# Kernel optimization log

Hardware: AMD Instinct MI355X
Metric: run time of the kernel (lower is better)

Reference implementation:

```python
import jax, jax.numpy as jnp
import numpy as np

DIM = 64


def setup_inputs() -> dict:
    key = jax.random.key(0)
    k1, k2, k3 = jax.random.split(key, 3)
    x = jax.random.normal(k1, (65536, DIM), dtype=jnp.float32)
    alpha = jax.random.uniform(k2, (), dtype=jnp.float32)
    beta = jax.random.uniform(k3, (), dtype=jnp.float32)
    return {"x": x, "alpha": alpha, "beta": beta}


def reference(x, alpha, beta):
    # Static upper-triangular index pairs (i < j), same as triu(...,1).nonzero()
    iu, ju = jnp.triu_indices(DIM, k=1)
    e = jnp.exp(-alpha * x)                 # [B, dim]
    # a[b, p] = exp(-alpha*x_i) - exp(-alpha*x_j) for each pair p=(i,j), i<j.
    # Equivalent to building the dense [B, dim, dim] tensor and gathering triu.
    a = e[..., iu] - e[..., ju]             # [B, dim*(dim-1)/2]
    log_vander = jnp.sum(jnp.log(jnp.abs(a)), axis=-1)  # [B]
    return 2.0 * (-beta * jnp.sum(x, axis=-1) + log_vander)
```

## Files before the change

kernel.cpp:

```cpp
#include <hip/hip_runtime.h>

#define DIM 64

__global__ __launch_bounds__(256) void vander_kernel(
    const float* __restrict__ x, const float* __restrict__ alpha,
    const float* __restrict__ beta, float* __restrict__ out, int nrows) {
  int row = blockIdx.x * blockDim.x + threadIdx.x;
  if (row >= nrows) return;

  const float c = -alpha[0] * 1.44269504088896340736f;
  const float b = beta[0];

  const float4* xr = reinterpret_cast<const float4*>(x) + row * (DIM / 4);

  float e[DIM];
  float xs = 0.f;
#pragma unroll
  for (int k = 0; k < DIM / 4; ++k) {
    float4 v = xr[k];
    xs += (v.x + v.y) + (v.z + v.w);
    e[4 * k + 0] = __builtin_amdgcn_exp2f(c * v.x);
    e[4 * k + 1] = __builtin_amdgcn_exp2f(c * v.y);
    e[4 * k + 2] = __builtin_amdgcn_exp2f(c * v.z);
    e[4 * k + 3] = __builtin_amdgcn_exp2f(c * v.w);
  }

  float accs[4] = {0.f, 0.f, 0.f, 0.f};
  float buf[4];
  int cnt = 0, g = 0;
#pragma unroll
  for (int i = 0; i < DIM; ++i) {
#pragma unroll
    for (int j = i + 1; j < DIM; ++j) {
      buf[cnt++] = e[i] - e[j];
      if (cnt == 4) {
        float p = (buf[0] * buf[1]) * (buf[2] * buf[3]);
        float ap = __builtin_fmaxf(__builtin_fabsf(p), 1e-37f);
        accs[g & 3] += __builtin_amdgcn_logf(ap);
        ++g;
        cnt = 0;
      }
    }
  }
  float lv = (accs[0] + accs[1]) + (accs[2] + accs[3]);
  out[row] = 2.0f * (-b * xs + 0.69314718055994530942f * lv);
}

extern "C" void kernel_launch(void* const* d_in, const int* in_sizes, int n_in,
                              void* d_out, int out_size, void* d_ws, size_t ws_size,
                              hipStream_t stream) {
  const float* x = (const float*)d_in[0];
  const float* alpha = (const float*)d_in[1];
  const float* beta = (const float*)d_in[2];
  float* out = (float*)d_out;
  int nrows = in_sizes[0] / DIM;
  int block = 256;
  int grid = (nrows + block - 1) / block;
  hipLaunchKernelGGL(vander_kernel, dim3(grid), dim3(block), 0, stream,
                     x, alpha, beta, out, nrows);
}
```

Measured before the change: 76.57 us.

## Split each row's pair products across eight waves with folded triangular slices

```diff
diff --git a/kernel.cpp b/kernel.cpp
--- a/kernel.cpp
+++ b/kernel.cpp
@@ -2,17 +2,54 @@
 
 #define DIM 64
 
-__global__ __launch_bounds__(256) void vander_kernel(
+template <int A, int T>
+__device__ __forceinline__ float pdiff(const float (&e)[DIM]) {
+  constexpr int N1 = 63 - A;
+  constexpr int I = (T < N1) ? A : 62 - A;
+  constexpr int J = (T < N1) ? (A + 1 + T) : T;
+  return e[I] - e[J];
+}
+
+template <int A, int T, int NT>
+__device__ __forceinline__ void groups(const float (&e)[DIM], float& a0, float& a1) {
+  if constexpr (T < NT) {
+    float d0 = pdiff<A, T + 0>(e);
+    float d1 = pdiff<A, T + 1>(e);
+    float d2 = pdiff<A, T + 2>(e);
+    float d3 = pdiff<A, T + 3>(e);
+    float p = (d0 * d1) * (d2 * d3);
+    float ap = __builtin_fmaxf(__builtin_fabsf(p), 1e-37f);
+    if constexpr ((T & 4) == 0) {
+      a0 += __builtin_amdgcn_logf(ap);
+    } else {
+      a1 += __builtin_amdgcn_logf(ap);
+    }
+    groups<A, T + 4, NT>(e, a0, a1);
+  }
+}
+
+template <int W>
+__device__ __forceinline__ void do_slice(const float (&e)[DIM], float& a0, float& a1) {
+  groups<W, 0, 64>(e, a0, a1);
+  groups<W + 8, 0, 64>(e, a0, a1);
+  groups<W + 16, 0, 64>(e, a0, a1);
+  if constexpr (W + 24 < 31) {
+    groups<W + 24, 0, 64>(e, a0, a1);
+  } else {
+    groups<31, 0, 32>(e, a0, a1);
+  }
+}
+
+__global__ __launch_bounds__(512) void vander_kernel(
     const float* __restrict__ x, const float* __restrict__ alpha,
-    const float* __restrict__ beta, float* __restrict__ out, int nrows) {
-  int row = blockIdx.x * blockDim.x + threadIdx.x;
-  if (row >= nrows) return;
+    const float* __restrict__ beta, float* __restrict__ out) {
+  const int lane = threadIdx.x & 63;
+  const int w = threadIdx.x >> 6;
+  const int row = blockIdx.x * 64 + lane;
 
   const float c = -alpha[0] * 1.44269504088896340736f;
-  const float b = beta[0];
 
   const float4* xr = reinterpret_cast<const float4*>(x) + row * (DIM / 4);
-
   float e[DIM];
   float xs = 0.f;
 #pragma unroll
@@ -25,25 +62,27 @@
     e[4 * k + 3] = __builtin_amdgcn_exp2f(c * v.w);
   }
 
-  float accs[4] = {0.f, 0.f, 0.f, 0.f};
-  float buf[4];
-  int cnt = 0, g = 0;
-#pragma unroll
-  for (int i = 0; i < DIM; ++i) {
-#pragma unroll
-    for (int j = i + 1; j < DIM; ++j) {
-      buf[cnt++] = e[i] - e[j];
-      if (cnt == 4) {
-        float p = (buf[0] * buf[1]) * (buf[2] * buf[3]);
-        float ap = __builtin_fmaxf(__builtin_fabsf(p), 1e-37f);
-        accs[g & 3] += __builtin_amdgcn_logf(ap);
-        ++g;
-        cnt = 0;
-      }
-    }
+  float a0 = 0.f, a1 = 0.f;
+  switch (w) {
+    case 0: do_slice<0>(e, a0, a1); break;
+    case 1: do_slice<1>(e, a0, a1); break;
+    case 2: do_slice<2>(e, a0, a1); break;
+    case 3: do_slice<3>(e, a0, a1); break;
+    case 4: do_slice<4>(e, a0, a1); break;
+    case 5: do_slice<5>(e, a0, a1); break;
+    case 6: do_slice<6>(e, a0, a1); break;
+    default: do_slice<7>(e, a0, a1); break;
   }
-  float lv = (accs[0] + accs[1]) + (accs[2] + accs[3]);
-  out[row] = 2.0f * (-b * xs + 0.69314718055994530942f * lv);
+
+  __shared__ float ps[8][64];
+  ps[w][lane] = a0 + a1;
+  __syncthreads();
+
+  if (w == 0) {
+    float lv = ((ps[0][lane] + ps[1][lane]) + (ps[2][lane] + ps[3][lane])) +
+               ((ps[4][lane] + ps[5][lane]) + (ps[6][lane] + ps[7][lane]));
+    out[row] = 2.0f * (-beta[0] * xs + 0.69314718055994530942f * lv);
+  }
 }
 
 extern "C" void kernel_launch(void* const* d_in, const int* in_sizes, int n_in,
@@ -54,8 +93,7 @@
   const float* beta = (const float*)d_in[2];
   float* out = (float*)d_out;
   int nrows = in_sizes[0] / DIM;
-  int block = 256;
-  int grid = (nrows + block - 1) / block;
-  hipLaunchKernelGGL(vander_kernel, dim3(grid), dim3(block), 0, stream,
-                     x, alpha, beta, out, nrows);
+  int grid = nrows / 64;
+  hipLaunchKernelGGL(vander_kernel, dim3(grid), dim3(512), 0, stream,
+                     x, alpha, beta, out);
 }
```

Result: slower. 84.71 us (+10.6%).

## Split each row's pair-products across 8 waves via LDS tiles

Applied to the files above, without the earlier changes.

```diff
diff --git a/kernel.cpp b/kernel.cpp
--- a/kernel.cpp
+++ b/kernel.cpp
@@ -1,49 +1,125 @@
 #include <hip/hip_runtime.h>
 
-#define DIM 64
+#define STRIDE 66
 
-__global__ __launch_bounds__(256) void vander_kernel(
+typedef float v2f __attribute__((ext_vector_type(2)));
+
+__device__ __forceinline__ float lg(float p) {
+  return __builtin_amdgcn_logf(__builtin_fmaxf(__builtin_fabsf(p), 1e-37f));
+}
+
+__device__ __forceinline__ void load8(const float* p, float* r) {
+#pragma unroll
+  for (int k = 0; k < 4; ++k) {
+    float2 v = *reinterpret_cast<const float2*>(p + 2 * k);
+    r[2 * k] = v.x;
+    r[2 * k + 1] = v.y;
+  }
+}
+
+__device__ __forceinline__ void off8(const float* ei, const float* ej,
+                                     float& a0, float& a1) {
+  v2f e01 = {ej[0], ej[1]}, e23 = {ej[2], ej[3]};
+  v2f e45 = {ej[4], ej[5]}, e67 = {ej[6], ej[7]};
+#pragma unroll
+  for (int i = 0; i < 8; ++i) {
+    v2f b = {ei[i], ei[i]};
+    v2f d0 = b - e01, d1 = b - e23, d2 = b - e45, d3 = b - e67;
+    v2f p = d0 * d1, q = d2 * d3;
+    a0 += lg(p.x * p.y);
+    a1 += lg(q.x * q.y);
+  }
+}
+
+__device__ __forceinline__ void diag8(const float* e, float& a0, float& a1) {
+  a0 += lg(((e[0] - e[1]) * (e[0] - e[2])) * ((e[0] - e[3]) * (e[0] - e[4])));
+  a1 += lg(((e[0] - e[5]) * (e[0] - e[6])) * ((e[0] - e[7]) * (e[1] - e[2])));
+  a0 += lg(((e[1] - e[3]) * (e[1] - e[4])) * ((e[1] - e[5]) * (e[1] - e[6])));
+  a1 += lg(((e[1] - e[7]) * (e[2] - e[3])) * ((e[2] - e[4]) * (e[2] - e[5])));
+  a0 += lg(((e[2] - e[6]) * (e[2] - e[7])) * ((e[3] - e[4]) * (e[3] - e[5])));
+  a1 += lg(((e[3] - e[6]) * (e[3] - e[7])) * ((e[4] - e[5]) * (e[4] - e[6])));
+  a0 += lg(((e[4] - e[7]) * (e[5] - e[6])) * ((e[5] - e[7]) * (e[6] - e[7])));
+}
+
+__global__ __launch_bounds__(512, 6) void vander_kernel(
     const float* __restrict__ x, const float* __restrict__ alpha,
-    const float* __restrict__ beta, float* __restrict__ out, int nrows) {
-  int row = blockIdx.x * blockDim.x + threadIdx.x;
-  if (row >= nrows) return;
+    const float* __restrict__ beta, float* __restrict__ out) {
+  __shared__ float e_lds[64 * STRIDE];
+  __shared__ float xsum[512];
+  __shared__ float ps[512];
 
+  const int tid = threadIdx.x;
   const float c = -alpha[0] * 1.44269504088896340736f;
-  const float b = beta[0];
 
-  const float4* xr = reinterpret_cast<const float4*>(x) + row * (DIM / 4);
+  {
+    const float4* xp =
+        reinterpret_cast<const float4*>(x + (size_t)blockIdx.x * 4096 + tid * 8);
+    float4 u = xp[0], v = xp[1];
+    float ev[8];
+    ev[0] = __builtin_amdgcn_exp2f(c * u.x);
+    ev[1] = __builtin_amdgcn_exp2f(c * u.y);
+    ev[2] = __builtin_amdgcn_exp2f(c * u.z);
+    ev[3] = __builtin_amdgcn_exp2f(c * u.w);
+    ev[4] = __builtin_amdgcn_exp2f(c * v.x);
+    ev[5] = __builtin_amdgcn_exp2f(c * v.y);
+    ev[6] = __builtin_amdgcn_exp2f(c * v.z);
+    ev[7] = __builtin_amdgcn_exp2f(c * v.w);
+    float* ew = &e_lds[(tid >> 3) * STRIDE + (tid & 7) * 8];
+#pragma unroll
+    for (int k = 0; k < 4; ++k) {
+      float2 t;
+      t.x = ev[2 * k];
+      t.y = ev[2 * k + 1];
+      *reinterpret_cast<float2*>(ew + 2 * k) = t;
+    }
+    xsum[tid] = ((u.x + u.y) + (u.z + u.w)) + ((v.x + v.y) + (v.z + v.w));
+  }
+  __syncthreads();
 
-  float e[DIM];
-  float xs = 0.f;
+  const int lane = tid & 63;
+  const int w = tid >> 6;
+  const float* myrow = &e_lds[lane * STRIDE];
+  float a0 = 0.f, a1 = 0.f;
+
+  if (w < 6) {
+    int ti = (w < 3) ? 0 : ((w < 5) ? 1 : 2);
+    int tj = (w == 0) ? 1 : (w == 1) ? 2 : (w == 2) ? 3 : (w == 3) ? 2 : 3;
+    float ei[16], ej[16];
+    load8(myrow + ti * 16, ei);
+    load8(myrow + ti * 16 + 8, ei + 8);
+    load8(myrow + tj * 16, ej);
+    load8(myrow + tj * 16 + 8, ej + 8);
+    off8(ei, ej, a0, a1);
+    off8(ei, ej + 8, a0, a1);
+    off8(ei + 8, ej, a0, a1);
+    off8(ei + 8, ej + 8, a0, a1);
+  } else {
+    int d = (w - 6) * 2;
 #pragma unroll
-  for (int k = 0; k < DIM / 4; ++k) {
-    float4 v = xr[k];
-    xs += (v.x + v.y) + (v.z + v.w);
-    e[4 * k + 0] = __builtin_amdgcn_exp2f(c * v.x);
-    e[4 * k + 1] = __builtin_amdgcn_exp2f(c * v.y);
-    e[4 * k + 2] = __builtin_amdgcn_exp2f(c * v.z);
-    e[4 * k + 3] = __builtin_amdgcn_exp2f(c * v.w);
-  }
-
-  float accs[4] = {0.f, 0.f, 0.f, 0.f};
-  float buf[4];
-  int cnt = 0, g = 0;
-#pragma unroll
-  for (int i = 0; i < DIM; ++i) {
-#pragma unroll
-    for (int j = i + 1; j < DIM; ++j) {
-      buf[cnt++] = e[i] - e[j];
-      if (cnt == 4) {
-        float p = (buf[0] * buf[1]) * (buf[2] * buf[3]);
-        float ap = __builtin_fmaxf(__builtin_fabsf(p), 1e-37f);
-        accs[g & 3] += __builtin_amdgcn_logf(ap);
-        ++g;
-        cnt = 0;
-      }
+    for (int t = 0; t < 2; ++t) {
+      float ei[16];
+      load8(myrow + (d + t) * 16, ei);
+      load8(myrow + (d + t) * 16 + 8, ei + 8);
+      off8(ei, ei + 8, a0, a1);
+      diag8(ei, a0, a1);
+      diag8(ei + 8, a0, a1);
     }
   }
-  float lv = (accs[0] + accs[1]) + (accs[2] + accs[3]);
-  out[row] = 2.0f * (-b * xs + 0.69314718055994530942f * lv);
+  ps[lane * 8 + w] = a0 + a1;
+  __syncthreads();
+
+  if (w == 0) {
+    const float* pp = &ps[lane * 8];
+    const float* xq = &xsum[lane * 8];
+    float lv = 0.f, xs = 0.f;
+#pragma unroll
+    for (int k = 0; k < 8; ++k) {
+      lv += pp[k];
+      xs += xq[k];
+    }
+    out[blockIdx.x * 64 + lane] =
+        2.0f * (-beta[0] * xs + 0.69314718055994530942f * lv);
+  }
 }
 
 extern "C" void kernel_launch(void* const* d_in, const int* in_sizes, int n_in,
@@ -53,9 +129,8 @@
   const float* alpha = (const float*)d_in[1];
   const float* beta = (const float*)d_in[2];
   float* out = (float*)d_out;
-  int nrows = in_sizes[0] / DIM;
-  int block = 256;
-  int grid = (nrows + block - 1) / block;
-  hipLaunchKernelGGL(vander_kernel, dim3(grid), dim3(block), 0, stream,
-                     x, alpha, beta, out, nrows);
+  int nrows = in_sizes[0] / 64;
+  int grid = nrows / 64;
+  hipLaunchKernelGGL(vander_kernel, dim3(grid), dim3(512), 0, stream,
+                     x, alpha, beta, out);
 }
```

New measurement: 71.62 us. 1.07x faster.

## Split each row's pairwise work across four waves via LDS-staged exponentials

Applied to the files above, without the earlier changes.

```diff
diff --git a/kernel.cpp b/kernel.cpp
--- a/kernel.cpp
+++ b/kernel.cpp
@@ -1,49 +1,120 @@
 #include <hip/hip_runtime.h>
 
-#define DIM 64
+#define STRIDE 66
+
+typedef float v2f __attribute__((ext_vector_type(2)));
+
+__constant__ unsigned char CI[28] = {0,0,0,0,0,0,0, 1,1,1,1,1,1, 2,2,2,2,2, 3,3,3,3, 4,4,4, 5,5, 6};
+__constant__ unsigned char CJ[28] = {1,2,3,4,5,6,7, 2,3,4,5,6,7, 3,4,5,6,7, 4,5,6,7, 5,6,7, 6,7, 7};
+
+__device__ __forceinline__ float lg(float p) {
+  return __builtin_amdgcn_logf(__builtin_fmaxf(__builtin_fabsf(p), 1e-37f));
+}
+
+struct E8 { v2f a, b, c, d; };
+
+__device__ __forceinline__ E8 load8(const float* p) {
+  E8 r;
+  r.a = *reinterpret_cast<const v2f*>(p);
+  r.b = *reinterpret_cast<const v2f*>(p + 2);
+  r.c = *reinterpret_cast<const v2f*>(p + 4);
+  r.d = *reinterpret_cast<const v2f*>(p + 6);
+  return r;
+}
+
+__device__ __forceinline__ void cross1(float b, const E8& ej, float& a0, float& a1) {
+  v2f bb = {b, b};
+  v2f d0 = bb - ej.a, d1 = bb - ej.b, d2 = bb - ej.c, d3 = bb - ej.d;
+  v2f p = d0 * d1, q = d2 * d3;
+  a0 += lg(p.x * p.y);
+  a1 += lg(q.x * q.y);
+}
+
+__device__ __forceinline__ void cross8(const E8& ei, const E8& ej, float& a0, float& a1) {
+  cross1(ei.a.x, ej, a0, a1); cross1(ei.a.y, ej, a0, a1);
+  cross1(ei.b.x, ej, a0, a1); cross1(ei.b.y, ej, a0, a1);
+  cross1(ei.c.x, ej, a0, a1); cross1(ei.c.y, ej, a0, a1);
+  cross1(ei.d.x, ej, a0, a1); cross1(ei.d.y, ej, a0, a1);
+}
+
+__device__ __forceinline__ void diag8(const E8& e, float& a0, float& a1) {
+  float e0 = e.a.x, e1 = e.a.y, e2 = e.b.x, e3 = e.b.y;
+  float e4 = e.c.x, e5 = e.c.y, e6 = e.d.x, e7 = e.d.y;
+  a0 += lg(((e0 - e1) * (e0 - e2)) * ((e0 - e3) * (e0 - e4)));
+  a1 += lg(((e0 - e5) * (e0 - e6)) * ((e0 - e7) * (e1 - e2)));
+  a0 += lg(((e1 - e3) * (e1 - e4)) * ((e1 - e5) * (e1 - e6)));
+  a1 += lg(((e1 - e7) * (e2 - e3)) * ((e2 - e4) * (e2 - e5)));
+  a0 += lg(((e2 - e6) * (e2 - e7)) * ((e3 - e4) * (e3 - e5)));
+  a1 += lg(((e3 - e6) * (e3 - e7)) * ((e4 - e5) * (e4 - e6)));
+  a0 += lg(((e4 - e7) * (e5 - e6)) * ((e5 - e7) * (e6 - e7)));
+}
 
 __global__ __launch_bounds__(256) void vander_kernel(
     const float* __restrict__ x, const float* __restrict__ alpha,
-    const float* __restrict__ beta, float* __restrict__ out, int nrows) {
-  int row = blockIdx.x * blockDim.x + threadIdx.x;
-  if (row >= nrows) return;
+    const float* __restrict__ beta, float* __restrict__ out) {
+  __shared__ float e_lds[64 * STRIDE];
+  __shared__ float xsum[256];
+  __shared__ float ps[64 * 4];
 
+  const int tid = threadIdx.x;
   const float c = -alpha[0] * 1.44269504088896340736f;
-  const float b = beta[0];
 
-  const float4* xr = reinterpret_cast<const float4*>(x) + row * (DIM / 4);
+  {
+    const float4* xp = reinterpret_cast<const float4*>(x) +
+                       (size_t)blockIdx.x * 1024 + tid * 4;
+    float4 u0 = xp[0], u1 = xp[1], u2 = xp[2], u3 = xp[3];
+    float* ew = &e_lds[(tid >> 2) * STRIDE + (tid & 3) * 16];
+    v2f t;
+    t.x = __builtin_amdgcn_exp2f(c * u0.x); t.y = __builtin_amdgcn_exp2f(c * u0.y);
+    *reinterpret_cast<v2f*>(ew + 0) = t;
+    t.x = __builtin_amdgcn_exp2f(c * u0.z); t.y = __builtin_amdgcn_exp2f(c * u0.w);
+    *reinterpret_cast<v2f*>(ew + 2) = t;
+    t.x = __builtin_amdgcn_exp2f(c * u1.x); t.y = __builtin_amdgcn_exp2f(c * u1.y);
+    *reinterpret_cast<v2f*>(ew + 4) = t;
+    t.x = __builtin_amdgcn_exp2f(c * u1.z); t.y = __builtin_amdgcn_exp2f(c * u1.w);
+    *reinterpret_cast<v2f*>(ew + 6) = t;
+    t.x = __builtin_amdgcn_exp2f(c * u2.x); t.y = __builtin_amdgcn_exp2f(c * u2.y);
+    *reinterpret_cast<v2f*>(ew + 8) = t;
+    t.x = __builtin_amdgcn_exp2f(c * u2.z); t.y = __builtin_amdgcn_exp2f(c * u2.w);
+    *reinterpret_cast<v2f*>(ew + 10) = t;
+    t.x = __builtin_amdgcn_exp2f(c * u3.x); t.y = __builtin_amdgcn_exp2f(c * u3.y);
+    *reinterpret_cast<v2f*>(ew + 12) = t;
+    t.x = __builtin_amdgcn_exp2f(c * u3.z); t.y = __builtin_amdgcn_exp2f(c * u3.w);
+    *reinterpret_cast<v2f*>(ew + 14) = t;
+    xsum[tid] = (((u0.x + u0.y) + (u0.z + u0.w)) + ((u1.x + u1.y) + (u1.z + u1.w))) +
+                (((u2.x + u2.y) + (u2.z + u2.w)) + ((u3.x + u3.y) + (u3.z + u3.w)));
+  }
+  __syncthreads();
 
-  float e[DIM];
-  float xs = 0.f;
-#pragma unroll
-  for (int k = 0; k < DIM / 4; ++k) {
-    float4 v = xr[k];
-    xs += (v.x + v.y) + (v.z + v.w);
-    e[4 * k + 0] = __builtin_amdgcn_exp2f(c * v.x);
-    e[4 * k + 1] = __builtin_amdgcn_exp2f(c * v.y);
-    e[4 * k + 2] = __builtin_amdgcn_exp2f(c * v.z);
-    e[4 * k + 3] = __builtin_amdgcn_exp2f(c * v.w);
+  const int lane = tid & 63;
+  const int w = tid >> 6;
+  const float* myrow = &e_lds[lane * STRIDE];
+  float a0 = 0.f, a1 = 0.f;
+
+#pragma unroll 1
+  for (int t = 0; t < 7; ++t) {
+    int k = w * 7 + t;
+    int ci = CI[k], cj = CJ[k];
+    E8 ei = load8(myrow + ci * 8);
+    E8 ej = load8(myrow + cj * 8);
+    cross8(ei, ej, a0, a1);
   }
+#pragma unroll 1
+  for (int t = 0; t < 2; ++t) {
+    E8 ed = load8(myrow + (w * 2 + t) * 8);
+    diag8(ed, a0, a1);
+  }
+  ps[lane * 4 + w] = a0 + a1;
+  __syncthreads();
 
-  float accs[4] = {0.f, 0.f, 0.f, 0.f};
-  float buf[4];
-  int cnt = 0, g = 0;
-#pragma unroll
-  for (int i = 0; i < DIM; ++i) {
-#pragma unroll
-    for (int j = i + 1; j < DIM; ++j) {
-      buf[cnt++] = e[i] - e[j];
-      if (cnt == 4) {
-        float p = (buf[0] * buf[1]) * (buf[2] * buf[3]);
-        float ap = __builtin_fmaxf(__builtin_fabsf(p), 1e-37f);
-        accs[g & 3] += __builtin_amdgcn_logf(ap);
-        ++g;
-        cnt = 0;
-      }
-    }
+  if (w == 0) {
+    const float* pp = &ps[lane * 4];
+    const float* xq = &xsum[lane * 4];
+    float lv = (pp[0] + pp[1]) + (pp[2] + pp[3]);
+    float xs = (xq[0] + xq[1]) + (xq[2] + xq[3]);
+    out[blockIdx.x * 64 + lane] =
+        2.0f * (-beta[0] * xs + 0.69314718055994530942f * lv);
   }
-  float lv = (accs[0] + accs[1]) + (accs[2] + accs[3]);
-  out[row] = 2.0f * (-b * xs + 0.69314718055994530942f * lv);
 }
 
 extern "C" void kernel_launch(void* const* d_in, const int* in_sizes, int n_in,
@@ -53,9 +124,8 @@
   const float* alpha = (const float*)d_in[1];
   const float* beta = (const float*)d_in[2];
   float* out = (float*)d_out;
-  int nrows = in_sizes[0] / DIM;
-  int block = 256;
-  int grid = (nrows + block - 1) / block;
-  hipLaunchKernelGGL(vander_kernel, dim3(grid), dim3(block), 0, stream,
-                     x, alpha, beta, out, nrows);
+  int nrows = in_sizes[0] / 64;
+  int grid = nrows / 64;
+  hipLaunchKernelGGL(vander_kernel, dim3(grid), dim3(256), 0, stream,
+                     x, alpha, beta, out);
 }
```

Result: faster. 73.54 us (-4.0%).
